# Kernel optimization log

Measured on AMD Instinct MI355X. Metric: run time of the kernel, lower is better.

Reference implementation:

```python
import jax, jax.numpy as jnp
import numpy as np
from jax.experimental import sparse as jsparse

N_ITEMS = 20000   # item catalog size (S is [N_ITEMS, N_ITEMS])
N_USERS = 2048    # user batch
NNZ = 4_000_000


def setup_inputs() -> dict:
    key = jax.random.key(0)
    k1, k2, k3, k4 = jax.random.split(key, 4)
    X = jax.random.normal(k1, (N_USERS, N_ITEMS), dtype=jnp.float32)
    S_vals = jax.random.normal(k2, (NNZ,), dtype=jnp.float32)
    S_rows = jax.random.randint(k3, (NNZ,), 0, N_ITEMS, dtype=jnp.int32)
    S_cols = jax.random.randint(k4, (NNZ,), 0, N_ITEMS, dtype=jnp.int32)
    return {"X": X, "S_vals": S_vals, "S_rows": S_rows, "S_cols": S_cols}


def reference(X, S_vals, S_rows, S_cols):
    # torch.sparse.mm(S, X.t()).t()  ==  X @ S^T, with S sparse COO.
    indices = jnp.stack([S_rows, S_cols], axis=1)  # [nnz, 2]
    S = jsparse.BCOO((S_vals, indices), shape=(N_ITEMS, N_ITEMS))
    # (S @ X^T)^T -> [n_users, n_items]; duplicate indices sum, matching COO semantics.
    return (S @ X.T).T
```

## Files before the change

kernel.cpp:

```cpp
#include <hip/hip_runtime.h>

#define N_ITEMS 20000
#define N_USERS 2048
#define NNZ     4000000
#define LDP     2112
#define CAP     320

typedef float    f32x4 __attribute__((ext_vector_type(4)));
typedef unsigned u32x4 __attribute__((ext_vector_type(4)));

#define OFF_XT     ((size_t)0)
#define OFF_CSRPK  ((size_t)84480000)
#define OFF_CNT    (OFF_CSRPK + 25600000)

static __device__ __forceinline__ unsigned short f2bf(float f) {
  unsigned u = __float_as_uint(f);
  unsigned r = (u + 0x7fffu + ((u >> 16) & 1u)) >> 16;
  return (unsigned short)r;
}

#define NT_BLOCKS (313 * 32)
#define NS_BLOCKS ((NNZ / 4 + 255) / 256)

__global__ __launch_bounds__(256) void prep_kernel(
    const float* __restrict__ X, const float* __restrict__ vals,
    const int* __restrict__ rows, const int* __restrict__ cols,
    unsigned short* __restrict__ XT, int* __restrict__ cnt,
    unsigned* __restrict__ csr_pk) {
  int b = blockIdx.x;
  if (b < NT_BLOCKS) {
    __shared__ float tile[64][65];
    int k0 = (b % 313) * 64;
    int u0 = (b / 313) * 64;
    int lane = threadIdx.x & 63;
    int dq = threadIdx.x >> 6;
    #pragma unroll
    for (int m = 0; m < 16; ++m) {
      int u = u0 + dq + 4 * m;
      int k = k0 + lane;
      float v = 0.f;
      if (k < N_ITEMS) v = X[(size_t)u * N_ITEMS + k];
      tile[lane][dq + 4 * m] = v;
    }
    __syncthreads();
    #pragma unroll
    for (int m = 0; m < 16; ++m) {
      int k = k0 + dq + 4 * m;
      if (k < N_ITEMS)
        XT[(size_t)k * LDP + u0 + lane] = f2bf(tile[dq + 4 * m][lane]);
    }
  } else {
    int i = ((b - NT_BLOCKS) * 256 + threadIdx.x) * 4;
    if (i < NNZ) {
      int4   r4 = *reinterpret_cast<const int4*>(rows + i);
      int4   c4 = *reinterpret_cast<const int4*>(cols + i);
      float4 v4 = *reinterpret_cast<const float4*>(vals + i);
      #pragma unroll
      for (int k = 0; k < 4; ++k) {
        int   r = (k == 0) ? r4.x : (k == 1) ? r4.y : (k == 2) ? r4.z : r4.w;
        int   c = (k == 0) ? c4.x : (k == 1) ? c4.y : (k == 2) ? c4.z : c4.w;
        float v = (k == 0) ? v4.x : (k == 1) ? v4.y : (k == 2) ? v4.z : v4.w;
        int pos = atomicAdd(&cnt[r], 1);
        if (pos >= CAP) pos = CAP - 1;
        csr_pk[r * CAP + pos] = ((unsigned)c << 16) | (unsigned)f2bf(v);
      }
    }
  }
}

__global__ __launch_bounds__(256) void spmm_kernel(
    const int* __restrict__ cnt, const unsigned* __restrict__ csr_pk,
    const unsigned short* __restrict__ xt, float* __restrict__ out) {
  __shared__ float tile[16][132];
  int wg = blockIdx.x;
  int xcd = wg & 7;
  int slot = wg >> 3;
  int combo = slot / 1250;
  int rb = slot - combo * 1250;
  int uchunk = xcd * 2 + combo;
  int u0 = uchunk * 128;
  int r0 = rb * 16;
  int lane = threadIdx.x & 63;
  int wave = __builtin_amdgcn_readfirstlane((int)(threadIdx.x >> 6));
  const char* xtb = (const char*)(xt + u0);
  unsigned lane4 = 4 * (unsigned)lane;

#define LOAD8(E, BASE)                                                   \
  { u32x4 q0 = *reinterpret_cast<const u32x4*>(csr_pk + (BASE));         \
    u32x4 q1 = *reinterpret_cast<const u32x4*>(csr_pk + (BASE) + 4);     \
    E[0] = q0.x; E[1] = q0.y; E[2] = q0.z; E[3] = q0.w;                  \
    E[4] = q1.x; E[5] = q1.y; E[6] = q1.z; E[7] = q1.w; }
#define GATHER8(G, E)                                                    \
  { _Pragma("unroll")                                                    \
    for (int k = 0; k < 8; ++k)                                          \
      G[k] = *reinterpret_cast<const unsigned*>(                         \
          xtb + ((E[k] >> 16) * (unsigned)(LDP * 2) + lane4)); }
#define FMA8(G, E)                                                       \
  { _Pragma("unroll")                                                    \
    for (int k = 0; k < 8; ++k) {                                        \
      float v  = __uint_as_float(E[k] << 16);            \
      float xl = __uint_as_float(G[k] << 16);                            \
      float xh = __uint_as_float(G[k]);             \
      if (k & 1) { a2 = fmaf(v, xl, a2); a3 = fmaf(v, xh, a3); }         \
      else       { a0 = fmaf(v, xl, a0); a1 = fmaf(v, xh, a1); }         \
    } }

  #pragma unroll 1
  for (int rr = 0; rr < 4; ++rr) {
    int r = r0 + wave * 4 + rr;
    int jb = r * CAP;
    int cr = __builtin_amdgcn_readfirstlane(cnt[r]);
    if (cr > CAP) cr = CAP;
    int nb = (cr + 7) >> 3;
    float a0 = 0.f, a1 = 0.f, a2 = 0.f, a3 = 0.f;
    if (nb >= 3) {
      unsigned e0[8], e1[8], e2[8], g0[8], g1[8], g2[8];
      LOAD8(e0, jb)
      GATHER8(g0, e0)
      LOAD8(e1, jb + 8)
      GATHER8(g1, e1)
      LOAD8(e2, jb + 16)
      int b = 0;
      for (; b + 5 < nb; b += 3) {
        GATHER8(g2, e2)
        FMA8(g0, e0)
        LOAD8(e0, jb + (b + 3) * 8)
        GATHER8(g0, e0)
        FMA8(g1, e1)
        LOAD8(e1, jb + (b + 4) * 8)
        GATHER8(g1, e1)
        FMA8(g2, e2)
        LOAD8(e2, jb + (b + 5) * 8)
      }
      int m = nb - b;
      GATHER8(g2, e2)
      FMA8(g0, e0)
      if (m == 3) {
        FMA8(g1, e1)
        FMA8(g2, e2)
      } else if (m == 4) {
        LOAD8(e0, jb + (b + 3) * 8)
        GATHER8(g0, e0)
        FMA8(g1, e1)
        FMA8(g2, e2)
        FMA8(g0, e0)
      } else {
        LOAD8(e0, jb + (b + 3) * 8)
        GATHER8(g0, e0)
        FMA8(g1, e1)
        LOAD8(e1, jb + (b + 4) * 8)
        GATHER8(g1, e1)
        FMA8(g2, e2)
        FMA8(g0, e0)
        FMA8(g1, e1)
      }
    } else if (nb == 2) {
      unsigned e0[8], e1[8], g0[8], g1[8];
      LOAD8(e0, jb)
      GATHER8(g0, e0)
      LOAD8(e1, jb + 8)
      GATHER8(g1, e1)
      FMA8(g0, e0)
      FMA8(g1, e1)
    } else if (nb == 1) {
      unsigned e0[8], g0[8];
      LOAD8(e0, jb)
      GATHER8(g0, e0)
      FMA8(g0, e0)
    }
    tile[wave * 4 + rr][2 * lane]     = a0 + a2;
    tile[wave * 4 + rr][2 * lane + 1] = a1 + a3;
  }
#undef LOAD8
#undef GATHER8
#undef FMA8

  __syncthreads();
  int ul = threadIdx.x >> 1;
  int rseg = (threadIdx.x & 1) * 8;
  float* op = &out[(size_t)(u0 + ul) * N_ITEMS + r0 + rseg];
  f32x4 o0, o1;
  o0.x = tile[rseg + 0][ul]; o0.y = tile[rseg + 1][ul];
  o0.z = tile[rseg + 2][ul]; o0.w = tile[rseg + 3][ul];
  o1.x = tile[rseg + 4][ul]; o1.y = tile[rseg + 5][ul];
  o1.z = tile[rseg + 6][ul]; o1.w = tile[rseg + 7][ul];
  __builtin_nontemporal_store(o0, reinterpret_cast<f32x4*>(op));
  __builtin_nontemporal_store(o1, reinterpret_cast<f32x4*>(op) + 1);
}

extern "C" void kernel_launch(void* const* d_in, const int* in_sizes, int n_in,
                              void* d_out, int out_size, void* d_ws, size_t ws_size,
                              hipStream_t stream) {
  const float* X      = (const float*)d_in[0];
  const float* S_vals = (const float*)d_in[1];
  const int*   S_rows = (const int*)d_in[2];
  const int*   S_cols = (const int*)d_in[3];
  float* out = (float*)d_out;

  char* ws = (char*)d_ws;
  unsigned short* XT = (unsigned short*)(ws + OFF_XT);
  unsigned* csr_pk   = (unsigned*)(ws + OFF_CSRPK);
  int* cnt           = (int*)(ws + OFF_CNT);

  hipMemsetAsync(cnt, 0, N_ITEMS * sizeof(int), stream);
  hipMemsetAsync(csr_pk, 0, (size_t)N_ITEMS * CAP * sizeof(unsigned), stream);
  prep_kernel<<<NT_BLOCKS + NS_BLOCKS, 256, 0, stream>>>(
      X, S_vals, S_rows, S_cols, XT, cnt, csr_pk);
  spmm_kernel<<<1250 * 16, 256, 0, stream>>>(cnt, csr_pk, XT, out);
}
```

Measured before the change: 1.092 ms.

## Split COO scatter into two row-half passes and use nontemporal loads/stores in prep

```diff
diff --git a/kernel.cpp b/kernel.cpp
--- a/kernel.cpp
+++ b/kernel.cpp
@@ -4,9 +4,11 @@
 #define N_USERS 2048
 #define NNZ     4000000
 #define LDP     2112
+#define HALF_ITEMS 10000
 #define CAP     320
 
 typedef float    f32x4 __attribute__((ext_vector_type(4)));
+typedef int      i32x4 __attribute__((ext_vector_type(4)));
 typedef unsigned u32x4 __attribute__((ext_vector_type(4)));
 
 #define OFF_XT     ((size_t)0)
@@ -19,19 +21,50 @@
   return (unsigned short)r;
 }
 
+#define NSQ ((NNZ / 4 + 255) / 256)
 #define NT_BLOCKS (313 * 32)
-#define NS_BLOCKS ((NNZ / 4 + 255) / 256)
-
-__global__ __launch_bounds__(256) void prep_kernel(
-    const float* __restrict__ X, const float* __restrict__ vals,
+
+static __device__ __forceinline__ void scatter_body(
     const int* __restrict__ rows, const int* __restrict__ cols,
+    const float* __restrict__ vals, int* __restrict__ cnt,
+    unsigned* __restrict__ csr_pk, int pass, int b) {
+  int i = (b * 256 + (int)threadIdx.x) * 4;
+  if (i < NNZ) {
+    i32x4 r4 = __builtin_nontemporal_load(reinterpret_cast<const i32x4*>(rows + i));
+    i32x4 c4 = __builtin_nontemporal_load(reinterpret_cast<const i32x4*>(cols + i));
+    f32x4 v4 = __builtin_nontemporal_load(reinterpret_cast<const f32x4*>(vals + i));
+    #pragma unroll
+    for (int k = 0; k < 4; ++k) {
+      int r = r4[k];
+      if ((unsigned)(r - pass * HALF_ITEMS) < (unsigned)HALF_ITEMS) {
+        int pos = atomicAdd(&cnt[r], 1);
+        if (pos >= CAP) pos = CAP - 1;
+        csr_pk[r * CAP + pos] = ((unsigned)c4[k] << 16) | (unsigned)f2bf(v4[k]);
+      }
+    }
+  }
+}
+
+__global__ __launch_bounds__(256) void scatterA_kernel(
+    const int* __restrict__ rows, const int* __restrict__ cols,
+    const float* __restrict__ vals, int* __restrict__ cnt,
+    unsigned* __restrict__ csr_pk) {
+  scatter_body(rows, cols, vals, cnt, csr_pk, 0, blockIdx.x);
+}
+
+__global__ __launch_bounds__(256) void prepB_kernel(
+    const float* __restrict__ X, const int* __restrict__ rows,
+    const int* __restrict__ cols, const float* __restrict__ vals,
     unsigned short* __restrict__ XT, int* __restrict__ cnt,
     unsigned* __restrict__ csr_pk) {
   int b = blockIdx.x;
-  if (b < NT_BLOCKS) {
+  if (b < NSQ) {
+    scatter_body(rows, cols, vals, cnt, csr_pk, 1, b);
+  } else {
     __shared__ float tile[64][65];
-    int k0 = (b % 313) * 64;
-    int u0 = (b / 313) * 64;
+    int b2 = b - NSQ;
+    int k0 = (b2 % 313) * 64;
+    int u0 = (b2 / 313) * 64;
     int lane = threadIdx.x & 63;
     int dq = threadIdx.x >> 6;
     #pragma unroll
@@ -39,30 +72,17 @@
       int u = u0 + dq + 4 * m;
       int k = k0 + lane;
       float v = 0.f;
-      if (k < N_ITEMS) v = X[(size_t)u * N_ITEMS + k];
+      if (k < N_ITEMS)
+        v = __builtin_nontemporal_load(&X[(size_t)u * N_ITEMS + k]);
       tile[lane][dq + 4 * m] = v;
     }
     __syncthreads();
     #pragma unroll
     for (int m = 0; m < 16; ++m) {
       int k = k0 + dq + 4 * m;
-      if (k < N_ITEMS)
-        XT[(size_t)k * LDP + u0 + lane] = f2bf(tile[dq + 4 * m][lane]);
-    }
-  } else {
-    int i = ((b - NT_BLOCKS) * 256 + threadIdx.x) * 4;
-    if (i < NNZ) {
-      int4   r4 = *reinterpret_cast<const int4*>(rows + i);
-      int4   c4 = *reinterpret_cast<const int4*>(cols + i);
-      float4 v4 = *reinterpret_cast<const float4*>(vals + i);
-      #pragma unroll
-      for (int k = 0; k < 4; ++k) {
-        int   r = (k == 0) ? r4.x : (k == 1) ? r4.y : (k == 2) ? r4.z : r4.w;
-        int   c = (k == 0) ? c4.x : (k == 1) ? c4.y : (k == 2) ? c4.z : c4.w;
-        float v = (k == 0) ? v4.x : (k == 1) ? v4.y : (k == 2) ? v4.z : v4.w;
-        int pos = atomicAdd(&cnt[r], 1);
-        if (pos >= CAP) pos = CAP - 1;
-        csr_pk[r * CAP + pos] = ((unsigned)c << 16) | (unsigned)f2bf(v);
+      if (k < N_ITEMS) {
+        unsigned short s = f2bf(tile[dq + 4 * m][lane]);
+        __builtin_nontemporal_store(s, &XT[(size_t)k * LDP + u0 + lane]);
       }
     }
   }
@@ -204,7 +224,8 @@
 
   hipMemsetAsync(cnt, 0, N_ITEMS * sizeof(int), stream);
   hipMemsetAsync(csr_pk, 0, (size_t)N_ITEMS * CAP * sizeof(unsigned), stream);
-  prep_kernel<<<NT_BLOCKS + NS_BLOCKS, 256, 0, stream>>>(
-      X, S_vals, S_rows, S_cols, XT, cnt, csr_pk);
+  scatterA_kernel<<<NSQ, 256, 0, stream>>>(S_rows, S_cols, S_vals, cnt, csr_pk);
+  prepB_kernel<<<NSQ + NT_BLOCKS, 256, 0, stream>>>(
+      X, S_rows, S_cols, S_vals, XT, cnt, csr_pk);
   spmm_kernel<<<1250 * 16, 256, 0, stream>>>(cnt, csr_pk, XT, out);
 }
```

Measured after the change: 1.071 ms. No clear change (-1.9%).
